# Optimization experiments

Measured on AMD Instinct MI355X. Metric: run time of the kernel, lower is better.

The kernel has to match this reference:

```python
import jax, jax.numpy as jnp
import numpy as np

NB_LAYERS, KSIZE = 4, 5
DILATIONS = [1, 2, 4, 8]
NEG_SLOPE = 0.1
BN_EPS = 1e-5


def _cont_conv(times, feats, mask, dilation, p):
    """One ContConv1d layer: causal gather of time-diffs -> kernel MLP -> weighted aggregate + skip + BN."""
    k1W, k1b, k2W, k2b, k3W, k3b, skipW, skipb, gamma, beta = p
    bs, L, Cin = feats.shape
    Cout = skipW.shape[1]
    lags = jnp.arange(KSIZE) * dilation                    # (K,) include_zero_lag=True -> lag 0 included
    idx = jnp.arange(L)[None, :] - lags[:, None]           # (K, L) causal neighbor indices
    valid = idx >= 0
    idx_c = jnp.clip(idx, 0, L - 1)
    g_times = times[:, idx_c]                              # (bs, K, L)
    g_feats = feats[:, idx_c, :]                           # (bs, K, L, Cin)
    g_mask = (mask[:, idx_c] & valid[None] & mask[:, None, :]).astype(feats.dtype)
    dt = (times[:, None, :] - g_times) * g_mask            # (bs, K, L) zeroed where invalid
    # kernel MLP: scalar time-diff -> (Cin, Cout) mixing matrix
    h = jax.nn.leaky_relu(dt[..., None] @ k1W + k1b, NEG_SLOPE)
    h = jax.nn.leaky_relu(h @ k2W + k2b, NEG_SLOPE)
    kv = (h @ k3W + k3b).reshape(bs, KSIZE, L, Cin, Cout) * g_mask[..., None, None]
    out = jnp.einsum('bklc,bklcd->bld', g_feats, kv)       # aggregate over taps and input channels
    out = out + feats @ skipW + skipb                      # 1x1-conv skip connection
    mu = out.mean((0, 1))                                  # BatchNorm1d (training-mode batch stats)
    var = out.var((0, 1))
    return (out - mu) * jax.lax.rsqrt(var + BN_EPS) * gamma + beta


def _ccnn_forward(event_times, event_types, emb, k1W, k1b, k2W, k2b, k3W, k3b, skipW, skipb, gamma, beta):
    bs = event_times.shape[0]
    emb = emb.at[0].set(0.0)                               # padding_idx = 0
    times = jnp.concatenate([jnp.zeros((bs, 1), event_times.dtype), event_times], axis=1)
    bos = jnp.full((bs, 1), jnp.max(event_types) + 1, dtype=event_types.dtype)
    types = jnp.concatenate([bos, event_types], axis=1)
    mask = times != 0                                      # BOS (t=0) masked, as in the original
    enc = emb[types]                                       # (bs, L+1, C)
    for i in range(NB_LAYERS):
        p = (k1W[i], k1b[i], k2W[i], k2b[i], k3W[i], k3b[i], skipW[i], skipb[i], gamma[i], beta[i])
        enc = jax.nn.leaky_relu(_cont_conv(times, enc, mask, DILATIONS[i], p), NEG_SLOPE)
    return enc


def setup_inputs() -> dict:
    key = jax.random.key(0)
    ks = jax.random.split(key, 12)
    bs, L, C, H, num_types = 8, 2048, 32, 16, 100
    s = 0.05
    gaps = jax.random.uniform(ks[0], (bs, L)) * 0.1 + 0.01
    times = jnp.cumsum(gaps, axis=1)                       # strictly increasing positive event times
    types = jax.random.randint(ks[1], (bs, L), 0, num_types) + 1   # 1..num_types
    pad = jnp.arange(L) >= int(0.9 * L)
    times = jnp.where(pad[None, :], 0.0, times).astype(jnp.float32)
    types = jnp.where(pad[None, :], 0, types).astype(jnp.int32)
    return {
        'event_times': times,
        'event_types': types,
        'emb': jax.random.normal(ks[2], (num_types + 2, C)) * s,
        'k1W': jax.random.normal(ks[3], (NB_LAYERS, 1, H)) * s,
        'k1b': jnp.zeros((NB_LAYERS, H)),
        'k2W': jax.random.normal(ks[4], (NB_LAYERS, H, H)) * s,
        'k2b': jnp.zeros((NB_LAYERS, H)),
        'k3W': jax.random.normal(ks[5], (NB_LAYERS, H, C * C)) * s,
        'k3b': jnp.zeros((NB_LAYERS, C * C)),
        'skipW': jax.random.normal(ks[6], (NB_LAYERS, C, C)) * s,
        'skipb': jnp.zeros((NB_LAYERS, C)),
        'gamma': jnp.ones((NB_LAYERS, C)),
        'beta': jnp.zeros((NB_LAYERS, C)),
    }


def reference(event_times, event_types, emb, k1W, k1b, k2W, k2b, k3W, k3b, skipW, skipb, gamma, beta):
    return _ccnn_forward(event_times, event_types, emb, k1W, k1b, k2W, k2b, k3W, k3b, skipW, skipb, gamma, beta)
```

## Files before the change

kernel.cpp:

```cpp
#include <hip/hip_runtime.h>
#include <stdint.h>

#define NB_LAYERS 4
#define KSIZE 5
#define BSZ 8
#define LIN 2048
#define LSEQ 2049
#define CCH 32
#define HCH 16
#define MROWS (BSZ*LSEQ)
#define NTILES ((MROWS+15)/16)
#define KDIM 576
#define NEG 0.1f
#define BNEPS 1e-5f

typedef _Float16 h2v __attribute__((ext_vector_type(2)));
typedef _Float16 h8v __attribute__((ext_vector_type(8)));
typedef float    f4v __attribute__((ext_vector_type(4)));

union H8 { h8v v; h2v h[4]; };

static __device__ __forceinline__ h2v mkh2(float a, float b) {
  h2v r; r[0] = (_Float16)a; r[1] = (_Float16)b; return r;
}

__global__ void init_kernel(float* stats, int* maxp) {
  int i = blockIdx.x * blockDim.x + threadIdx.x;
  if (i < NB_LAYERS * 64) stats[i] = 0.f;
  if (i == 0) *maxp = 0;
}

__global__ void max_kernel(const int* __restrict__ types, int* maxp) {
  int i = blockIdx.x * blockDim.x + threadIdx.x;
  int v = 0;
  if (i < BSZ * LIN) v = types[i];
#pragma unroll
  for (int off = 32; off; off >>= 1) v = max(v, __shfl_xor(v, off, 64));
  if ((threadIdx.x & 63) == 0) atomicMax(maxp, v);
}

__global__ void prep_kernel(const float* __restrict__ k3W, const float* __restrict__ k3b,
                            const float* __restrict__ skipW, _Float16* __restrict__ Wt) {
  int id = blockIdx.x * blockDim.x + threadIdx.x;
  if (id >= NB_LAYERS * CCH * KDIM) return;
  int layer = id / (CCH * KDIM);
  int rem = id % (CCH * KDIM);
  int n = rem / KDIM;
  int k = rem % KDIM;
  float val;
  if (k < 512)      { int h = k >> 5, c = k & 31; val = k3W[layer*16384 + h*1024 + c*32 + n]; }
  else if (k < 544) { int c = k - 512;            val = k3b[layer*1024 + c*32 + n]; }
  else              { int c = k - 544;            val = skipW[layer*1024 + c*32 + n]; }
  Wt[id] = (_Float16)val;
}

__global__ void embed_kernel(const int* __restrict__ types, const float* __restrict__ emb,
                             const int* __restrict__ maxp, float* __restrict__ enc) {
  int id = blockIdx.x * blockDim.x + threadIdx.x;
  if (id >= MROWS * CCH) return;
  int row = id >> 5, c = id & 31;
  int b = row / LSEQ, pos = row % LSEQ;
  int t = (pos == 0) ? (*maxp + 1) : types[b * LIN + pos - 1];
  enc[id] = (t == 0) ? 0.f : emb[t * CCH + c];
}

__global__ __launch_bounds__(256) void conv_kernel(
    const float* __restrict__ enc_in, float* __restrict__ enc_out,
    const float* __restrict__ etimes,
    const float* __restrict__ k1Wp, const float* __restrict__ k1bp,
    const float* __restrict__ k2Wp, const float* __restrict__ k2bp,
    const _Float16* __restrict__ Wt,
    float* __restrict__ stats, int dil)
{
  __shared__ float sst[64];
  if (threadIdx.x < 64) sst[threadIdx.x] = 0.f;
  __syncthreads();

  const int lane = threadIdx.x & 63;
  const int wv   = threadIdx.x >> 6;
  const int m    = lane & 15;
  const int q    = lane >> 4;

  float k1w[HCH], k1b[HCH], k2b[HCH];
#pragma unroll
  for (int h = 0; h < HCH; h++) { k1w[h] = k1Wp[h]; k1b[h] = k1bp[h]; k2b[h] = k2bp[h]; }

  const _Float16* wb0 = Wt + m * KDIM + q * 8;
  const _Float16* wb1 = Wt + (m + 16) * KDIM + q * 8;

  for (int tile = blockIdx.x * 4 + wv; tile < NTILES; tile += gridDim.x * 4) {
    int row = tile * 16 + m;
    bool rvalid = row < MROWS;
    int rowc = min(row, MROWS - 1);
    int b = rowc / LSEQ, pos = rowc % LSEQ;
    float t_l = (pos == 0) ? 0.f : etimes[b * LIN + pos - 1];
    bool mask_l = rvalid && (t_l != 0.f);

    h2v wh[KSIZE][8];
    h2v fh[KSIZE][4];
    h2v fself[4];
    float Fb[8];
#pragma unroll
    for (int jj = 0; jj < 8; jj++) Fb[jj] = 0.f;

#pragma unroll
    for (int tap = 0; tap < KSIZE; tap++) {
      int j = pos - tap * dil;
      int jc = max(j, 0);
      float t_j = (jc == 0) ? 0.f : etimes[b * LIN + jc - 1];
      bool gm = mask_l && (j >= 0) && (t_j != 0.f);
      float dt = gm ? (t_l - t_j) : 0.f;

      const float* fp = enc_in + (b * LSEQ + jc) * CCH + q * 8;
      float4 fA = *(const float4*)(fp);
      float4 fB = *(const float4*)(fp + 4);
      float fv[8] = {fA.x, fA.y, fA.z, fA.w, fB.x, fB.y, fB.z, fB.w};

      if (tap == 0) {
        float rv = rvalid ? 1.f : 0.f;
#pragma unroll
        for (int p = 0; p < 4; p++) fself[p] = mkh2(fv[2*p] * rv, fv[2*p+1] * rv);
      }
      float g = gm ? 1.f : 0.f;
#pragma unroll
      for (int jj = 0; jj < 8; jj++) Fb[jj] += g * fv[jj];
#pragma unroll
      for (int p = 0; p < 4; p++) fh[tap][p] = mkh2(fv[2*p], fv[2*p+1]);

      if (__ballot(gm)) {
        float h1[HCH];
#pragma unroll
        for (int h = 0; h < HCH; h++) { float x = fmaf(dt, k1w[h], k1b[h]); h1[h] = fmaxf(x, NEG * x); }
        float h2[HCH];
#pragma unroll
        for (int h = 0; h < HCH; h++) h2[h] = k2b[h];
#pragma unroll
        for (int hp = 0; hp < HCH; hp++) {
          float hv = h1[hp];
#pragma unroll
          for (int h = 0; h < HCH; h++) h2[h] = fmaf(hv, k2Wp[hp * HCH + h], h2[h]);
        }
#pragma unroll
        for (int hh = 0; hh < 8; hh++) {
          float a = h2[2*hh];     a = fmaxf(a, NEG * a) * g;
          float c2 = h2[2*hh+1];  c2 = fmaxf(c2, NEG * c2) * g;
          wh[tap][hh] = mkh2(a, c2);
        }
      } else {
#pragma unroll
        for (int hh = 0; hh < 8; hh++) wh[tap][hh] = mkh2(0.f, 0.f);
      }
    }

    f4v acc0 = {0.f, 0.f, 0.f, 0.f};
    f4v acc1 = {0.f, 0.f, 0.f, 0.f};

#pragma unroll
    for (int ks = 0; ks < 16; ks++) {
      H8 bf0, bf1, af;
      bf0.v = *(const h8v*)(wb0 + ks * 32);
      bf1.v = *(const h8v*)(wb1 + ks * 32);
      h2v u0 = mkh2(0.f,0.f), u1 = mkh2(0.f,0.f), u2 = mkh2(0.f,0.f), u3 = mkh2(0.f,0.f);
#pragma unroll
      for (int tap = 0; tap < KSIZE; tap++) {
        _Float16 w = wh[tap][ks >> 1][ks & 1];
        h2v wd; wd[0] = w; wd[1] = w;
        u0 += wd * fh[tap][0];
        u1 += wd * fh[tap][1];
        u2 += wd * fh[tap][2];
        u3 += wd * fh[tap][3];
      }
      af.h[0] = u0; af.h[1] = u1; af.h[2] = u2; af.h[3] = u3;
      acc0 = __builtin_amdgcn_mfma_f32_16x16x32_f16(af.v, bf0.v, acc0, 0, 0, 0);
      acc1 = __builtin_amdgcn_mfma_f32_16x16x32_f16(af.v, bf1.v, acc1, 0, 0, 0);
    }
    {
      H8 bf0, bf1, af;
      bf0.v = *(const h8v*)(wb0 + 512);
      bf1.v = *(const h8v*)(wb1 + 512);
#pragma unroll
      for (int p = 0; p < 4; p++) af.h[p] = mkh2(Fb[2*p], Fb[2*p+1]);
      acc0 = __builtin_amdgcn_mfma_f32_16x16x32_f16(af.v, bf0.v, acc0, 0, 0, 0);
      acc1 = __builtin_amdgcn_mfma_f32_16x16x32_f16(af.v, bf1.v, acc1, 0, 0, 0);
    }
    {
      H8 bf0, bf1, af;
      bf0.v = *(const h8v*)(wb0 + 544);
      bf1.v = *(const h8v*)(wb1 + 544);
      af.h[0] = fself[0]; af.h[1] = fself[1]; af.h[2] = fself[2]; af.h[3] = fself[3];
      acc0 = __builtin_amdgcn_mfma_f32_16x16x32_f16(af.v, bf0.v, acc0, 0, 0, 0);
      acc1 = __builtin_amdgcn_mfma_f32_16x16x32_f16(af.v, bf1.v, acc1, 0, 0, 0);
    }

    float s0 = 0.f, s1 = 0.f, s2 = 0.f, s3 = 0.f;
#pragma unroll
    for (int r = 0; r < 4; r++) {
      float v0 = acc0[r], v1 = acc1[r];
      s0 += v0; s1 += v0 * v0; s2 += v1; s3 += v1 * v1;
      int rd = tile * 16 + q * 4 + r;
      if (rd < MROWS) {
        enc_out[rd * CCH + m] = v0;
        enc_out[rd * CCH + 16 + m] = v1;
      }
    }
    s0 += __shfl_xor(s0, 16, 64); s0 += __shfl_xor(s0, 32, 64);
    s1 += __shfl_xor(s1, 16, 64); s1 += __shfl_xor(s1, 32, 64);
    s2 += __shfl_xor(s2, 16, 64); s2 += __shfl_xor(s2, 32, 64);
    s3 += __shfl_xor(s3, 16, 64); s3 += __shfl_xor(s3, 32, 64);
    if (q == 0) {
      atomicAdd(&sst[m], s0);
      atomicAdd(&sst[32 + m], s1);
      atomicAdd(&sst[16 + m], s2);
      atomicAdd(&sst[48 + m], s3);
    }
  }
  __syncthreads();
  if (threadIdx.x < 64) atomicAdd(&stats[threadIdx.x], sst[threadIdx.x]);
}

__global__ void bn_kernel(const float* __restrict__ x, float* __restrict__ out,
                          const float* __restrict__ stats,
                          const float* __restrict__ gamma, const float* __restrict__ beta) {
  int id = blockIdx.x * blockDim.x + threadIdx.x;
  if (id >= MROWS * CCH) return;
  int c = id & 31;
  const float inv = 1.f / (float)MROWS;
  float mu = stats[c] * inv;
  float var = stats[32 + c] * inv - mu * mu;
  float sc = gamma[c] * rsqrtf(var + BNEPS);
  float v = (x[id] - mu) * sc + beta[c];
  out[id] = fmaxf(v, NEG * v);
}

extern "C" void kernel_launch(void* const* d_in, const int* in_sizes, int n_in,
                              void* d_out, int out_size, void* d_ws, size_t ws_size,
                              hipStream_t stream) {
  (void)in_sizes; (void)n_in; (void)out_size; (void)ws_size;
  const float* event_times = (const float*)d_in[0];
  const int*   event_types = (const int*)d_in[1];
  const float* emb   = (const float*)d_in[2];
  const float* k1W   = (const float*)d_in[3];
  const float* k1b   = (const float*)d_in[4];
  const float* k2W   = (const float*)d_in[5];
  const float* k2b   = (const float*)d_in[6];
  const float* k3W   = (const float*)d_in[7];
  const float* k3b   = (const float*)d_in[8];
  const float* skipW = (const float*)d_in[9];
  const float* gamma = (const float*)d_in[11];
  const float* beta  = (const float*)d_in[12];

  float* enc_a = (float*)d_ws;
  float* enc_b = enc_a + (size_t)MROWS * CCH;
  float* stats = enc_b + (size_t)MROWS * CCH;
  int*   maxp  = (int*)(stats + NB_LAYERS * 64);
  _Float16* Wt = (_Float16*)(((uintptr_t)(maxp + 1) + 255) & ~(uintptr_t)255);

  init_kernel<<<2, 256, 0, stream>>>(stats, maxp);
  max_kernel<<<(BSZ * LIN + 255) / 256, 256, 0, stream>>>(event_types, maxp);
  prep_kernel<<<(NB_LAYERS * CCH * KDIM + 255) / 256, 256, 0, stream>>>(k3W, k3b, skipW, Wt);
  embed_kernel<<<(MROWS * CCH + 255) / 256, 256, 0, stream>>>(event_types, emb, maxp, enc_a);

  const int dils[NB_LAYERS] = {1, 2, 4, 8};
  for (int i = 0; i < NB_LAYERS; i++) {
    conv_kernel<<<256, 256, 0, stream>>>(enc_a, enc_b, event_times,
        k1W + i * HCH, k1b + i * HCH, k2W + i * HCH * HCH, k2b + i * HCH,
        Wt + (size_t)i * CCH * KDIM, stats + i * 64, dils[i]);
    float* nout = (i == NB_LAYERS - 1) ? (float*)d_out : enc_a;
    bn_kernel<<<(MROWS * CCH + 255) / 256, 256, 0, stream>>>(
        enc_b, nout, stats + i * 64, gamma + i * CCH, beta + i * CCH);
  }
}
```

Before: 177.7 us.

## Fuse all stages into one cooperative persistent kernel with BN folded into conv loads

Replaces the chain of separate init/max/prep/embed/conv/bn kernel launches with a single cooperative kernel that uses grid-wide syncs between stages. The BatchNorm plus leaky-ReLU of each layer is applied on the fly when the next conv layer loads its inputs, which removes the separate BN read/write passes. The grid is sized so each wave handles exactly one 16-row tile (205 blocks of 5 waves). The aim is to cut launch overhead and intermediate memory traffic. In exchange it adds grid barrier costs and recomputes BN per tap load.

Result: slower. 531.0 us (+198.9%).

```diff
diff --git a/kernel.cpp b/kernel.cpp
--- a/kernel.cpp
+++ b/kernel.cpp
@@ -1,5 +1,8 @@
 #include <hip/hip_runtime.h>
+#include <hip/hip_cooperative_groups.h>
 #include <stdint.h>
+
+namespace cg = cooperative_groups;
 
 #define NB_LAYERS 4
 #define KSIZE 5
@@ -13,6 +16,9 @@
 #define KDIM 576
 #define NEG 0.1f
 #define BNEPS 1e-5f
+#define GRID 205
+#define BLOCK 320
+#define NTHREADS (GRID*BLOCK)
 
 typedef _Float16 h2v __attribute__((ext_vector_type(2)));
 typedef _Float16 h8v __attribute__((ext_vector_type(8)));
@@ -24,55 +30,26 @@
   h2v r; r[0] = (_Float16)a; r[1] = (_Float16)b; return r;
 }
 
-__global__ void init_kernel(float* stats, int* maxp) {
-  int i = blockIdx.x * blockDim.x + threadIdx.x;
-  if (i < NB_LAYERS * 64) stats[i] = 0.f;
-  if (i == 0) *maxp = 0;
-}
-
-__global__ void max_kernel(const int* __restrict__ types, int* maxp) {
-  int i = blockIdx.x * blockDim.x + threadIdx.x;
-  int v = 0;
-  if (i < BSZ * LIN) v = types[i];
-#pragma unroll
-  for (int off = 32; off; off >>= 1) v = max(v, __shfl_xor(v, off, 64));
-  if ((threadIdx.x & 63) == 0) atomicMax(maxp, v);
-}
-
-__global__ void prep_kernel(const float* __restrict__ k3W, const float* __restrict__ k3b,
-                            const float* __restrict__ skipW, _Float16* __restrict__ Wt) {
-  int id = blockIdx.x * blockDim.x + threadIdx.x;
-  if (id >= NB_LAYERS * CCH * KDIM) return;
-  int layer = id / (CCH * KDIM);
-  int rem = id % (CCH * KDIM);
-  int n = rem / KDIM;
-  int k = rem % KDIM;
-  float val;
-  if (k < 512)      { int h = k >> 5, c = k & 31; val = k3W[layer*16384 + h*1024 + c*32 + n]; }
-  else if (k < 544) { int c = k - 512;            val = k3b[layer*1024 + c*32 + n]; }
-  else              { int c = k - 544;            val = skipW[layer*1024 + c*32 + n]; }
-  Wt[id] = (_Float16)val;
-}
-
-__global__ void embed_kernel(const int* __restrict__ types, const float* __restrict__ emb,
-                             const int* __restrict__ maxp, float* __restrict__ enc) {
-  int id = blockIdx.x * blockDim.x + threadIdx.x;
-  if (id >= MROWS * CCH) return;
-  int row = id >> 5, c = id & 31;
-  int b = row / LSEQ, pos = row % LSEQ;
-  int t = (pos == 0) ? (*maxp + 1) : types[b * LIN + pos - 1];
-  enc[id] = (t == 0) ? 0.f : emb[t * CCH + c];
-}
-
-__global__ __launch_bounds__(256) void conv_kernel(
+struct CParams {
+  const float* etimes; const int* types; const float* emb;
+  const float* k1W; const float* k1b; const float* k2W; const float* k2b;
+  const float* k3W; const float* k3b; const float* skipW;
+  const float* gamma; const float* beta;
+  float* enc_a; float* enc_b; float* stats; int* blockmax;
+  _Float16* Wt; float* out;
+};
+
+static __device__ __forceinline__ void gsync(cg::grid_group& g) {
+  __threadfence();
+  g.sync();
+  __threadfence();
+}
+
+template<bool FUSE_BN>
+static __device__ __forceinline__ void conv_layer(const CParams& P,
     const float* __restrict__ enc_in, float* __restrict__ enc_out,
-    const float* __restrict__ etimes,
-    const float* __restrict__ k1Wp, const float* __restrict__ k1bp,
-    const float* __restrict__ k2Wp, const float* __restrict__ k2bp,
-    const _Float16* __restrict__ Wt,
-    float* __restrict__ stats, int dil)
+    int layer, int dil, float* sst)
 {
-  __shared__ float sst[64];
   if (threadIdx.x < 64) sst[threadIdx.x] = 0.f;
   __syncthreads();
 
@@ -81,14 +58,39 @@
   const int m    = lane & 15;
   const int q    = lane >> 4;
 
+  const float* k1Wp = P.k1W + layer * HCH;
+  const float* k1bp = P.k1b + layer * HCH;
+  const float* k2Wp = P.k2W + layer * HCH * HCH;
+  const float* k2bp = P.k2b + layer * HCH;
+  const _Float16* Wt = P.Wt + (size_t)layer * CCH * KDIM;
+  float* stats_out = P.stats + layer * 64;
+  const float* etimes = P.etimes;
+
   float k1w[HCH], k1b[HCH], k2b[HCH];
 #pragma unroll
   for (int h = 0; h < HCH; h++) { k1w[h] = k1Wp[h]; k1b[h] = k1bp[h]; k2b[h] = k2bp[h]; }
+
+  float sc8[8], ob8[8];
+  if (FUSE_BN) {
+    const float* st = P.stats + (layer - 1) * 64;
+    const float* gm = P.gamma + (layer - 1) * CCH;
+    const float* bt = P.beta  + (layer - 1) * CCH;
+    const float inv = 1.f / (float)MROWS;
+#pragma unroll
+    for (int j = 0; j < 8; j++) {
+      int c = q * 8 + j;
+      float mu = st[c] * inv;
+      float var = st[32 + c] * inv - mu * mu;
+      float sc = gm[c] * rsqrtf(var + BNEPS);
+      sc8[j] = sc; ob8[j] = bt[c] - mu * sc;
+    }
+  }
 
   const _Float16* wb0 = Wt + m * KDIM + q * 8;
   const _Float16* wb1 = Wt + (m + 16) * KDIM + q * 8;
 
-  for (int tile = blockIdx.x * 4 + wv; tile < NTILES; tile += gridDim.x * 4) {
+  const int tile = blockIdx.x * (BLOCK / 64) + wv;
+  {
     int row = tile * 16 + m;
     bool rvalid = row < MROWS;
     int rowc = min(row, MROWS - 1);
@@ -115,17 +117,24 @@
       float4 fA = *(const float4*)(fp);
       float4 fB = *(const float4*)(fp + 4);
       float fv[8] = {fA.x, fA.y, fA.z, fA.w, fB.x, fB.y, fB.z, fB.w};
+      if (FUSE_BN) {
+#pragma unroll
+        for (int jj = 0; jj < 8; jj++) {
+          float x = fmaf(fv[jj], sc8[jj], ob8[jj]);
+          fv[jj] = fmaxf(x, NEG * x);
+        }
+      }
 
       if (tap == 0) {
         float rv = rvalid ? 1.f : 0.f;
 #pragma unroll
-        for (int p = 0; p < 4; p++) fself[p] = mkh2(fv[2*p] * rv, fv[2*p+1] * rv);
+        for (int p2 = 0; p2 < 4; p2++) fself[p2] = mkh2(fv[2*p2] * rv, fv[2*p2+1] * rv);
       }
       float g = gm ? 1.f : 0.f;
 #pragma unroll
       for (int jj = 0; jj < 8; jj++) Fb[jj] += g * fv[jj];
 #pragma unroll
-      for (int p = 0; p < 4; p++) fh[tap][p] = mkh2(fv[2*p], fv[2*p+1]);
+      for (int p2 = 0; p2 < 4; p2++) fh[tap][p2] = mkh2(fv[2*p2], fv[2*p2+1]);
 
       if (__ballot(gm)) {
         float h1[HCH];
@@ -179,7 +188,7 @@
       bf0.v = *(const h8v*)(wb0 + 512);
       bf1.v = *(const h8v*)(wb1 + 512);
 #pragma unroll
-      for (int p = 0; p < 4; p++) af.h[p] = mkh2(Fb[2*p], Fb[2*p+1]);
+      for (int p2 = 0; p2 < 4; p2++) af.h[p2] = mkh2(Fb[2*p2], Fb[2*p2+1]);
       acc0 = __builtin_amdgcn_mfma_f32_16x16x32_f16(af.v, bf0.v, acc0, 0, 0, 0);
       acc1 = __builtin_amdgcn_mfma_f32_16x16x32_f16(af.v, bf1.v, acc1, 0, 0, 0);
     }
@@ -215,58 +224,117 @@
     }
   }
   __syncthreads();
-  if (threadIdx.x < 64) atomicAdd(&stats[threadIdx.x], sst[threadIdx.x]);
-}
-
-__global__ void bn_kernel(const float* __restrict__ x, float* __restrict__ out,
-                          const float* __restrict__ stats,
-                          const float* __restrict__ gamma, const float* __restrict__ beta) {
-  int id = blockIdx.x * blockDim.x + threadIdx.x;
-  if (id >= MROWS * CCH) return;
-  int c = id & 31;
-  const float inv = 1.f / (float)MROWS;
-  float mu = stats[c] * inv;
-  float var = stats[32 + c] * inv - mu * mu;
-  float sc = gamma[c] * rsqrtf(var + BNEPS);
-  float v = (x[id] - mu) * sc + beta[c];
-  out[id] = fmaxf(v, NEG * v);
+  if (threadIdx.x < 64) atomicAdd(&stats_out[threadIdx.x], sst[threadIdx.x]);
+}
+
+__global__ __launch_bounds__(BLOCK, 1) void ccnn_kernel(CParams P) {
+  __shared__ float sst[64];
+  __shared__ int smax[BLOCK / 64];
+  cg::grid_group grid = cg::this_grid();
+
+  const int tid = threadIdx.x;
+  const int bid = blockIdx.x;
+  const int gtid = bid * BLOCK + tid;
+  const int lane = tid & 63;
+  const int wv = tid >> 6;
+
+  if (bid == 0 && tid < NB_LAYERS * 64) P.stats[tid] = 0.f;
+  {
+    int v = 0;
+    if (gtid < BSZ * LIN) v = P.types[gtid];
+#pragma unroll
+    for (int off = 32; off; off >>= 1) v = max(v, __shfl_xor(v, off, 64));
+    if (lane == 0) smax[wv] = v;
+  }
+  for (int id = gtid; id < NB_LAYERS * CCH * KDIM; id += NTHREADS) {
+    int layer = id / (CCH * KDIM);
+    int rem = id % (CCH * KDIM);
+    int n = rem / KDIM;
+    int k = rem % KDIM;
+    float val;
+    if (k < 512)      { int h = k >> 5, c = k & 31; val = P.k3W[layer*16384 + h*1024 + c*32 + n]; }
+    else if (k < 544) { int c = k - 512;            val = P.k3b[layer*1024 + c*32 + n]; }
+    else              { int c = k - 544;            val = P.skipW[layer*1024 + c*32 + n]; }
+    P.Wt[id] = (_Float16)val;
+  }
+  __syncthreads();
+  if (tid == 0) {
+    int v = smax[0];
+#pragma unroll
+    for (int i = 1; i < BLOCK / 64; i++) v = max(v, smax[i]);
+    P.blockmax[bid] = v;
+  }
+  gsync(grid);
+
+  {
+    int mx = -1;
+    for (int id = gtid; id < MROWS * CCH; id += NTHREADS) {
+      int row = id >> 5, c = id & 31;
+      int b = row / LSEQ, pos = row % LSEQ;
+      int t;
+      if (pos == 0) {
+        if (mx < 0) { mx = 0; for (int i = 0; i < GRID; i++) mx = max(mx, P.blockmax[i]); }
+        t = mx + 1;
+      } else {
+        t = P.types[b * LIN + pos - 1];
+      }
+      P.enc_a[id] = (t == 0) ? 0.f : P.emb[t * CCH + c];
+    }
+  }
+  gsync(grid);
+
+  conv_layer<false>(P, P.enc_a, P.enc_b, 0, 1, sst);
+  gsync(grid);
+  conv_layer<true >(P, P.enc_b, P.enc_a, 1, 2, sst);
+  gsync(grid);
+  conv_layer<true >(P, P.enc_a, P.enc_b, 2, 4, sst);
+  gsync(grid);
+  conv_layer<true >(P, P.enc_b, P.enc_a, 3, 8, sst);
+  gsync(grid);
+
+  {
+    const float* st = P.stats + 3 * 64;
+    const int c = gtid & 31;
+    const float inv = 1.f / (float)MROWS;
+    float mu = st[c] * inv;
+    float var = st[32 + c] * inv - mu * mu;
+    float sc = P.gamma[3 * CCH + c] * rsqrtf(var + BNEPS);
+    float ob = P.beta[3 * CCH + c] - mu * sc;
+    for (int id = gtid; id < MROWS * CCH; id += NTHREADS) {
+      float v = fmaf(P.enc_a[id], sc, ob);
+      P.out[id] = fmaxf(v, NEG * v);
+    }
+  }
 }
 
 extern "C" void kernel_launch(void* const* d_in, const int* in_sizes, int n_in,
                               void* d_out, int out_size, void* d_ws, size_t ws_size,
                               hipStream_t stream) {
   (void)in_sizes; (void)n_in; (void)out_size; (void)ws_size;
-  const float* event_times = (const float*)d_in[0];
-  const int*   event_types = (const int*)d_in[1];
-  const float* emb   = (const float*)d_in[2];
-  const float* k1W   = (const float*)d_in[3];
-  const float* k1b   = (const float*)d_in[4];
-  const float* k2W   = (const float*)d_in[5];
-  const float* k2b   = (const float*)d_in[6];
-  const float* k3W   = (const float*)d_in[7];
-  const float* k3b   = (const float*)d_in[8];
-  const float* skipW = (const float*)d_in[9];
-  const float* gamma = (const float*)d_in[11];
-  const float* beta  = (const float*)d_in[12];
+  CParams p;
+  p.etimes = (const float*)d_in[0];
+  p.types  = (const int*)d_in[1];
+  p.emb    = (const float*)d_in[2];
+  p.k1W    = (const float*)d_in[3];
+  p.k1b    = (const float*)d_in[4];
+  p.k2W    = (const float*)d_in[5];
+  p.k2b    = (const float*)d_in[6];
+  p.k3W    = (const float*)d_in[7];
+  p.k3b    = (const float*)d_in[8];
+  p.skipW  = (const float*)d_in[9];
+  p.gamma  = (const float*)d_in[11];
+  p.beta   = (const float*)d_in[12];
 
   float* enc_a = (float*)d_ws;
   float* enc_b = enc_a + (size_t)MROWS * CCH;
   float* stats = enc_b + (size_t)MROWS * CCH;
-  int*   maxp  = (int*)(stats + NB_LAYERS * 64);
-  _Float16* Wt = (_Float16*)(((uintptr_t)(maxp + 1) + 255) & ~(uintptr_t)255);
-
-  init_kernel<<<2, 256, 0, stream>>>(stats, maxp);
-  max_kernel<<<(BSZ * LIN + 255) / 256, 256, 0, stream>>>(event_types, maxp);
-  prep_kernel<<<(NB_LAYERS * CCH * KDIM + 255) / 256, 256, 0, stream>>>(k3W, k3b, skipW, Wt);
-  embed_kernel<<<(MROWS * CCH + 255) / 256, 256, 0, stream>>>(event_types, emb, maxp, enc_a);
-
-  const int dils[NB_LAYERS] = {1, 2, 4, 8};
-  for (int i = 0; i < NB_LAYERS; i++) {
-    conv_kernel<<<256, 256, 0, stream>>>(enc_a, enc_b, event_times,
-        k1W + i * HCH, k1b + i * HCH, k2W + i * HCH * HCH, k2b + i * HCH,
-        Wt + (size_t)i * CCH * KDIM, stats + i * 64, dils[i]);
-    float* nout = (i == NB_LAYERS - 1) ? (float*)d_out : enc_a;
-    bn_kernel<<<(MROWS * CCH + 255) / 256, 256, 0, stream>>>(
-        enc_b, nout, stats + i * 64, gamma + i * CCH, beta + i * CCH);
-  }
-}
+  int* blockmax = (int*)(stats + NB_LAYERS * 64);
+  _Float16* Wt = (_Float16*)(((uintptr_t)(blockmax + 256) + 255) & ~(uintptr_t)255);
+
+  p.enc_a = enc_a; p.enc_b = enc_b; p.stats = stats; p.blockmax = blockmax;
+  p.Wt = Wt; p.out = (float*)d_out;
+
+  void* kargs[] = { (void*)&p };
+  hipLaunchCooperativeKernel((const void*)ccnn_kernel, dim3(GRID), dim3(BLOCK),
+                             kargs, 0, stream);
+}
```

## Fuse batchnorm into next conv layer and merge setup kernels

Applied to the files above, without the earlier changes.

Applies the previous layer's BatchNorm and leaky ReLU on the fly inside the next conv kernel's gather, so the intermediate BN passes over the activation buffer disappear and only a final BN kernel remains. The init, max and prep kernels are merged into one launch that writes per-wave maxima, and the embed kernel reduces those maxima itself instead of relying on a global atomic. The conv grid becomes exactly one tile per wave (257 blocks), which removes the grid-stride loop. The cost is that BN math is recomputed once per gathered tap element, and exact grid sizes are now hard-coded to the problem shape.

Measured after the change: 166.7 us. 6.2% less time.

```diff
diff --git a/kernel.cpp b/kernel.cpp
--- a/kernel.cpp
+++ b/kernel.cpp
@@ -13,6 +13,7 @@
 #define KDIM 576
 #define NEG 0.1f
 #define BNEPS 1e-5f
+#define NWAVEMAX 256
 
 typedef _Float16 h2v __attribute__((ext_vector_type(2)));
 typedef _Float16 h8v __attribute__((ext_vector_type(8)));
@@ -24,53 +25,66 @@
   h2v r; r[0] = (_Float16)a; r[1] = (_Float16)b; return r;
 }
 
-__global__ void init_kernel(float* stats, int* maxp) {
-  int i = blockIdx.x * blockDim.x + threadIdx.x;
-  if (i < NB_LAYERS * 64) stats[i] = 0.f;
-  if (i == 0) *maxp = 0;
-}
-
-__global__ void max_kernel(const int* __restrict__ types, int* maxp) {
-  int i = blockIdx.x * blockDim.x + threadIdx.x;
-  int v = 0;
-  if (i < BSZ * LIN) v = types[i];
-#pragma unroll
-  for (int off = 32; off; off >>= 1) v = max(v, __shfl_xor(v, off, 64));
-  if ((threadIdx.x & 63) == 0) atomicMax(maxp, v);
-}
-
-__global__ void prep_kernel(const float* __restrict__ k3W, const float* __restrict__ k3b,
-                            const float* __restrict__ skipW, _Float16* __restrict__ Wt) {
+__global__ __launch_bounds__(256) void prep_kernel(
+    const float* __restrict__ k3W, const float* __restrict__ k3b,
+    const float* __restrict__ skipW, _Float16* __restrict__ Wt,
+    const int* __restrict__ types, int* __restrict__ wavemax,
+    float* __restrict__ stats) {
   int id = blockIdx.x * blockDim.x + threadIdx.x;
-  if (id >= NB_LAYERS * CCH * KDIM) return;
-  int layer = id / (CCH * KDIM);
-  int rem = id % (CCH * KDIM);
-  int n = rem / KDIM;
-  int k = rem % KDIM;
-  float val;
-  if (k < 512)      { int h = k >> 5, c = k & 31; val = k3W[layer*16384 + h*1024 + c*32 + n]; }
-  else if (k < 544) { int c = k - 512;            val = k3b[layer*1024 + c*32 + n]; }
-  else              { int c = k - 544;            val = skipW[layer*1024 + c*32 + n]; }
-  Wt[id] = (_Float16)val;
-}
-
-__global__ void embed_kernel(const int* __restrict__ types, const float* __restrict__ emb,
-                             const int* __restrict__ maxp, float* __restrict__ enc) {
+
+  if (id < NB_LAYERS * 64) stats[id] = 0.f;
+
+  if (id < BSZ * LIN) {
+    int v = types[id];
+#pragma unroll
+    for (int off = 32; off; off >>= 1) v = max(v, __shfl_xor(v, off, 64));
+    if ((threadIdx.x & 63) == 0) wavemax[id >> 6] = v;
+  }
+
+  {
+    int layer = id / (CCH * KDIM);
+    int rem = id % (CCH * KDIM);
+    int n = rem / KDIM;
+    int k = rem % KDIM;
+    float val;
+    if (k < 512)      { int h = k >> 5, c = k & 31; val = k3W[layer*16384 + h*1024 + c*32 + n]; }
+    else if (k < 544) { int c = k - 512;            val = k3b[layer*1024 + c*32 + n]; }
+    else              { int c = k - 544;            val = skipW[layer*1024 + c*32 + n]; }
+    Wt[id] = (_Float16)val;
+  }
+}
+
+__global__ __launch_bounds__(256) void embed_kernel(
+    const int* __restrict__ types, const float* __restrict__ emb,
+    const int* __restrict__ wavemax, float* __restrict__ enc) {
   int id = blockIdx.x * blockDim.x + threadIdx.x;
-  if (id >= MROWS * CCH) return;
   int row = id >> 5, c = id & 31;
   int b = row / LSEQ, pos = row % LSEQ;
-  int t = (pos == 0) ? (*maxp + 1) : types[b * LIN + pos - 1];
+  int t;
+  if (pos == 0) {
+    const int4* wm = (const int4*)wavemax;
+    int mx = 0;
+    for (int i = 0; i < NWAVEMAX / 4; i++) {
+      int4 v = wm[i];
+      mx = max(mx, max(max(v.x, v.y), max(v.z, v.w)));
+    }
+    t = mx + 1;
+  } else {
+    t = types[b * LIN + pos - 1];
+  }
   enc[id] = (t == 0) ? 0.f : emb[t * CCH + c];
 }
 
+template<bool FUSE_BN>
 __global__ __launch_bounds__(256) void conv_kernel(
     const float* __restrict__ enc_in, float* __restrict__ enc_out,
     const float* __restrict__ etimes,
     const float* __restrict__ k1Wp, const float* __restrict__ k1bp,
     const float* __restrict__ k2Wp, const float* __restrict__ k2bp,
     const _Float16* __restrict__ Wt,
-    float* __restrict__ stats, int dil)
+    const float* __restrict__ stats_prev, float* __restrict__ stats_out,
+    const float* __restrict__ gamma_prev, const float* __restrict__ beta_prev,
+    int dil)
 {
   __shared__ float sst[64];
   if (threadIdx.x < 64) sst[threadIdx.x] = 0.f;
@@ -85,10 +99,24 @@
 #pragma unroll
   for (int h = 0; h < HCH; h++) { k1w[h] = k1Wp[h]; k1b[h] = k1bp[h]; k2b[h] = k2bp[h]; }
 
+  float sc8[8], ob8[8];
+  if (FUSE_BN) {
+    const float inv = 1.f / (float)MROWS;
+#pragma unroll
+    for (int j = 0; j < 8; j++) {
+      int c = q * 8 + j;
+      float mu = stats_prev[c] * inv;
+      float var = stats_prev[32 + c] * inv - mu * mu;
+      float sc = gamma_prev[c] * rsqrtf(var + BNEPS);
+      sc8[j] = sc; ob8[j] = beta_prev[c] - mu * sc;
+    }
+  }
+
   const _Float16* wb0 = Wt + m * KDIM + q * 8;
   const _Float16* wb1 = Wt + (m + 16) * KDIM + q * 8;
 
-  for (int tile = blockIdx.x * 4 + wv; tile < NTILES; tile += gridDim.x * 4) {
+  const int tile = blockIdx.x * 4 + wv;
+  {
     int row = tile * 16 + m;
     bool rvalid = row < MROWS;
     int rowc = min(row, MROWS - 1);
@@ -115,17 +143,24 @@
       float4 fA = *(const float4*)(fp);
       float4 fB = *(const float4*)(fp + 4);
       float fv[8] = {fA.x, fA.y, fA.z, fA.w, fB.x, fB.y, fB.z, fB.w};
+      if (FUSE_BN) {
+#pragma unroll
+        for (int jj = 0; jj < 8; jj++) {
+          float x = fmaf(fv[jj], sc8[jj], ob8[jj]);
+          fv[jj] = fmaxf(x, NEG * x);
+        }
+      }
 
       if (tap == 0) {
         float rv = rvalid ? 1.f : 0.f;
 #pragma unroll
-        for (int p = 0; p < 4; p++) fself[p] = mkh2(fv[2*p] * rv, fv[2*p+1] * rv);
+        for (int p2 = 0; p2 < 4; p2++) fself[p2] = mkh2(fv[2*p2] * rv, fv[2*p2+1] * rv);
       }
       float g = gm ? 1.f : 0.f;
 #pragma unroll
       for (int jj = 0; jj < 8; jj++) Fb[jj] += g * fv[jj];
 #pragma unroll
-      for (int p = 0; p < 4; p++) fh[tap][p] = mkh2(fv[2*p], fv[2*p+1]);
+      for (int p2 = 0; p2 < 4; p2++) fh[tap][p2] = mkh2(fv[2*p2], fv[2*p2+1]);
 
       if (__ballot(gm)) {
         float h1[HCH];
@@ -179,7 +214,7 @@
       bf0.v = *(const h8v*)(wb0 + 512);
       bf1.v = *(const h8v*)(wb1 + 512);
 #pragma unroll
-      for (int p = 0; p < 4; p++) af.h[p] = mkh2(Fb[2*p], Fb[2*p+1]);
+      for (int p2 = 0; p2 < 4; p2++) af.h[p2] = mkh2(Fb[2*p2], Fb[2*p2+1]);
       acc0 = __builtin_amdgcn_mfma_f32_16x16x32_f16(af.v, bf0.v, acc0, 0, 0, 0);
       acc1 = __builtin_amdgcn_mfma_f32_16x16x32_f16(af.v, bf1.v, acc1, 0, 0, 0);
     }
@@ -215,20 +250,20 @@
     }
   }
   __syncthreads();
-  if (threadIdx.x < 64) atomicAdd(&stats[threadIdx.x], sst[threadIdx.x]);
-}
-
-__global__ void bn_kernel(const float* __restrict__ x, float* __restrict__ out,
-                          const float* __restrict__ stats,
-                          const float* __restrict__ gamma, const float* __restrict__ beta) {
+  if (threadIdx.x < 64) atomicAdd(&stats_out[threadIdx.x], sst[threadIdx.x]);
+}
+
+__global__ __launch_bounds__(256) void bn_kernel(
+    const float* __restrict__ x, float* __restrict__ out,
+    const float* __restrict__ stats,
+    const float* __restrict__ gamma, const float* __restrict__ beta) {
   int id = blockIdx.x * blockDim.x + threadIdx.x;
-  if (id >= MROWS * CCH) return;
   int c = id & 31;
   const float inv = 1.f / (float)MROWS;
   float mu = stats[c] * inv;
   float var = stats[32 + c] * inv - mu * mu;
   float sc = gamma[c] * rsqrtf(var + BNEPS);
-  float v = (x[id] - mu) * sc + beta[c];
+  float v = fmaf(x[id], sc, beta[c] - mu * sc);
   out[id] = fmaxf(v, NEG * v);
 }
 
@@ -252,21 +287,25 @@
   float* enc_a = (float*)d_ws;
   float* enc_b = enc_a + (size_t)MROWS * CCH;
   float* stats = enc_b + (size_t)MROWS * CCH;
-  int*   maxp  = (int*)(stats + NB_LAYERS * 64);
-  _Float16* Wt = (_Float16*)(((uintptr_t)(maxp + 1) + 255) & ~(uintptr_t)255);
-
-  init_kernel<<<2, 256, 0, stream>>>(stats, maxp);
-  max_kernel<<<(BSZ * LIN + 255) / 256, 256, 0, stream>>>(event_types, maxp);
-  prep_kernel<<<(NB_LAYERS * CCH * KDIM + 255) / 256, 256, 0, stream>>>(k3W, k3b, skipW, Wt);
-  embed_kernel<<<(MROWS * CCH + 255) / 256, 256, 0, stream>>>(event_types, emb, maxp, enc_a);
-
+  int*   wavemax = (int*)(stats + NB_LAYERS * 64);
+  _Float16* Wt = (_Float16*)(((uintptr_t)(wavemax + NWAVEMAX) + 255) & ~(uintptr_t)255);
+
+  prep_kernel<<<288, 256, 0, stream>>>(k3W, k3b, skipW, Wt, event_types, wavemax, stats);
+  embed_kernel<<<2049, 256, 0, stream>>>(event_types, emb, wavemax, enc_a);
+
+  conv_kernel<false><<<257, 256, 0, stream>>>(enc_a, enc_b, event_times,
+      k1W, k1b, k2W, k2b, Wt, nullptr, stats, nullptr, nullptr, 1);
   const int dils[NB_LAYERS] = {1, 2, 4, 8};
-  for (int i = 0; i < NB_LAYERS; i++) {
-    conv_kernel<<<256, 256, 0, stream>>>(enc_a, enc_b, event_times,
+  const float* bufs[2] = {enc_a, enc_b};
+  for (int i = 1; i < NB_LAYERS; i++) {
+    const float* cin = bufs[i & 1];
+    float* cout = (float*)bufs[(i + 1) & 1];
+    conv_kernel<true><<<257, 256, 0, stream>>>(cin, cout, event_times,
         k1W + i * HCH, k1b + i * HCH, k2W + i * HCH * HCH, k2b + i * HCH,
-        Wt + (size_t)i * CCH * KDIM, stats + i * 64, dils[i]);
-    float* nout = (i == NB_LAYERS - 1) ? (float*)d_out : enc_a;
-    bn_kernel<<<(MROWS * CCH + 255) / 256, 256, 0, stream>>>(
-        enc_b, nout, stats + i * 64, gamma + i * CCH, beta + i * CCH);
-  }
-}
+        Wt + (size_t)i * CCH * KDIM,
+        stats + (i - 1) * 64, stats + i * 64,
+        gamma + (i - 1) * CCH, beta + (i - 1) * CCH, dils[i]);
+  }
+  bn_kernel<<<2049, 256, 0, stream>>>(enc_a, (float*)d_out,
+      stats + 3 * 64, gamma + 3 * CCH, beta + 3 * CCH);
+}
```
